# Optimization experiments

Hardware: AMD Instinct MI355X
Metric: run time of the kernel (lower is better)

Reference implementation:

```python
import jax, jax.numpy as jnp
import numpy as np

SCALING = 2.0  # alpha / r = 128 / 64


def setup_inputs() -> dict:
    key = jax.random.key(0)
    k1, k2, k3, k4, k5 = jax.random.split(key, 5)
    B, S, DIN, DOUT, R = 4, 2048, 4096, 4096, 64
    x = jax.random.normal(k1, (B, S, DIN), dtype=jnp.float32)
    # int8 quantized weight codes in [-127, 127] (stored as int32 for portability)
    qweight = jax.random.randint(k2, (DOUT, DIN), -127, 128, dtype=jnp.int32)
    # per-output-row absmax dequant scale (already divided by 127)
    scale = jax.random.uniform(k3, (DOUT, 1), dtype=jnp.float32, minval=0.005, maxval=0.02)
    lora_A = jax.random.normal(k4, (R, DIN), dtype=jnp.float32) * 0.02
    lora_B = jax.random.normal(k5, (DOUT, R), dtype=jnp.float32) * 0.02
    return {"x": x, "qweight": qweight, "scale": scale, "lora_A": lora_A, "lora_B": lora_B}


def reference(x, qweight, scale, lora_A, lora_B):
    # inline int8 dequant: w[o,i] = code[o,i] * scale[o]
    w = qweight.astype(x.dtype) * scale  # [DOUT, DIN]
    base = jnp.einsum('bsi,oi->bso', x, w)
    # low-rank LoRA path: (x @ A^T) @ B^T, scaled
    xa = jnp.einsum('bsi,ri->bsr', x, lora_A)       # [B,S,R]
    lora = jnp.einsum('bsr,or->bso', xa, lora_B)    # [B,S,DOUT]
    return base + SCALING * lora
```

## Files before the change

### kernel.cpp

```cpp
#include <hip/hip_runtime.h>
#include <hip/hip_bf16.h>
#include <stdint.h>


typedef __bf16 bf16x8 __attribute__((ext_vector_type(8)));
typedef float f32x4 __attribute__((ext_vector_type(4)));
typedef int i32x4 __attribute__((ext_vector_type(4)));

#define DIN   4096
#define DOUT  4096
#define MTOT  8192
#define RNK   64
#define NT    64
#define BUFB  24576

__device__ inline void gload_lds16(const void* g, void* l) {
  __builtin_amdgcn_global_load_lds((const __attribute__((address_space(1))) void*)g,
                                   (__attribute__((address_space(3))) void*)l,
                                   16, 0, 0);
}

__global__ __launch_bounds__(256) void quant_x_kernel(const float* __restrict__ x,
                                                      signed char* __restrict__ Xi8,
                                                      float* __restrict__ tstep) {
  const int row = blockIdx.x, t = threadIdx.x;
  const float4* xr = (const float4*)(x + (size_t)row * DIN);
  float4 v[4];
  float m = 0.f;
#pragma unroll
  for (int s = 0; s < 4; ++s) {
    v[s] = xr[t + s * 256];
    m = fmaxf(m, fmaxf(fmaxf(fabsf(v[s].x), fabsf(v[s].y)),
                       fmaxf(fabsf(v[s].z), fabsf(v[s].w))));
  }
#pragma unroll
  for (int off = 32; off > 0; off >>= 1) m = fmaxf(m, __shfl_xor(m, off));
  __shared__ float wm[4];
  if ((t & 63) == 0) wm[t >> 6] = m;
  __syncthreads();
  m = fmaxf(fmaxf(wm[0], wm[1]), fmaxf(wm[2], wm[3]));
  m = fmaxf(m, 1e-30f);
  const float rs = 127.0f / m;
  int* orow = (int*)(Xi8 + (size_t)row * DIN);
#pragma unroll
  for (int s = 0; s < 4; ++s) {
    float e[4] = {v[s].x, v[s].y, v[s].z, v[s].w};
    union { signed char c[4]; int i; } p;
#pragma unroll
    for (int j = 0; j < 4; ++j) {
      int q = __float2int_rn(e[j] * rs);
      q = q > 127 ? 127 : (q < -127 ? -127 : q);
      p.c[j] = (signed char)q;
    }
    orow[t + s * 256] = p.i;
  }
  if (t == 0) tstep[row] = m * (1.0f / 127.0f);
}

__global__ void cvt_w_kernel(const int* __restrict__ q, signed char* __restrict__ Wi8) {
  int i = blockIdx.x * blockDim.x + threadIdx.x;
  int4 v = ((const int4*)q)[i];
  union { signed char c[4]; int i; } p;
  p.c[0] = (signed char)v.x; p.c[1] = (signed char)v.y;
  p.c[2] = (signed char)v.z; p.c[3] = (signed char)v.w;
  ((int*)Wi8)[i] = p.i;
}

__global__ __launch_bounds__(256) void cvt_ab_kernel(const float* __restrict__ A,
                                                     const float* __restrict__ B,
                                                     signed char* __restrict__ Ai8,
                                                     float* __restrict__ astep,
                                                     __bf16* __restrict__ Blt) {
  const int t = threadIdx.x;
  if (blockIdx.x < 64) {
    const int row = blockIdx.x;
    const float4* ar = (const float4*)(A + (size_t)row * DIN);
    float4 v[4];
    float m = 0.f;
#pragma unroll
    for (int s = 0; s < 4; ++s) {
      v[s] = ar[t + s * 256];
      m = fmaxf(m, fmaxf(fmaxf(fabsf(v[s].x), fabsf(v[s].y)),
                         fmaxf(fabsf(v[s].z), fabsf(v[s].w))));
    }
#pragma unroll
    for (int off = 32; off > 0; off >>= 1) m = fmaxf(m, __shfl_xor(m, off));
    __shared__ float wm[4];
    if ((t & 63) == 0) wm[t >> 6] = m;
    __syncthreads();
    m = fmaxf(fmaxf(wm[0], wm[1]), fmaxf(wm[2], wm[3]));
    m = fmaxf(m, 1e-30f);
    const float rs = 127.0f / m;
    int* orow = (int*)(Ai8 + (size_t)row * DIN);
#pragma unroll
    for (int s = 0; s < 4; ++s) {
      float e[4] = {v[s].x, v[s].y, v[s].z, v[s].w};
      union { signed char c[4]; int i; } p;
#pragma unroll
      for (int j = 0; j < 4; ++j) {
        int q = __float2int_rn(e[j] * rs);
        q = q > 127 ? 127 : (q < -127 ? -127 : q);
        p.c[j] = (signed char)q;
      }
      orow[t + s * 256] = p.i;
    }
    if (t == 0) astep[row] = m * (1.0f / 127.0f);
  } else {
    int i = (blockIdx.x - 64) * 256 + t;
    float4 v = ((const float4*)B)[i];
    union { __bf16 h[4]; uint64_t u; } p;
    p.h[0] = (__bf16)(2.0f * v.x); p.h[1] = (__bf16)(2.0f * v.y);
    p.h[2] = (__bf16)(2.0f * v.z); p.h[3] = (__bf16)(2.0f * v.w);
    ((uint64_t*)Blt)[i] = p.u;
  }
}

__global__ __launch_bounds__(128) void lora_xa_kernel(const signed char* __restrict__ Xi8,
                                                      const float* __restrict__ tstep,
                                                      const signed char* __restrict__ Ai8,
                                                      const float* __restrict__ astep,
                                                      __bf16* __restrict__ xa) {
  int wid = threadIdx.x >> 6, lane = threadIdx.x & 63;
  int rowbase = blockIdx.x * 32 + wid * 16;
  i32x4 acc[4] = {};
  const signed char* xrow = Xi8 + (size_t)(rowbase + (lane & 15)) * DIN + (lane >> 4) * 16;
  const signed char* ab = Ai8 + (size_t)(lane & 15) * DIN + (lane >> 4) * 16;
  for (int k0 = 0; k0 < DIN; k0 += 64) {
    i32x4 af = *(const i32x4*)(xrow + k0);
#pragma unroll
    for (int ni = 0; ni < 4; ++ni) {
      i32x4 bv = *(const i32x4*)(ab + (size_t)ni * 16 * DIN + k0);
      acc[ni] = __builtin_amdgcn_mfma_i32_16x16x64_i8(af, bv, acc[ni], 0, 0, 0);
    }
  }
  f32x4 tm = *(const f32x4*)&tstep[rowbase + (lane >> 4) * 4];
#pragma unroll
  for (int ni = 0; ni < 4; ++ni) {
    const int col = ni * 16 + (lane & 15);
    const float as = astep[col];
#pragma unroll
    for (int j = 0; j < 4; ++j) {
      int row = rowbase + (lane >> 4) * 4 + j;
      xa[(size_t)row * RNK + col] = (__bf16)((float)acc[ni][j] * tm[j] * as);
    }
  }
}

__global__ __launch_bounds__(512, 4) void gemm_i8_kernel(const signed char* __restrict__ Xi8,
                                                         const signed char* __restrict__ Wi8,
                                                         const float* __restrict__ scale,
                                                         const float* __restrict__ tstep,
                                                         const __bf16* __restrict__ xa,
                                                         const __bf16* __restrict__ Blt,
                                                         float* __restrict__ out) {
  extern __shared__ char smem[];
  const int tid = threadIdx.x;
  const int lane = tid & 63;
  const int w = tid >> 6;
  const int wr = w >> 2;
  const int wc = w & 3;

  const int swz = (blockIdx.x & 7) * 128 + (blockIdx.x >> 3);
  const int bx = swz & 15;
  const int by = swz >> 4;
  const size_t bm = (size_t)by * 128, bn = (size_t)bx * 256;

  const int rc = ((lane >> 4) ^ ((lane >> 1) & 3)) << 4;
  const int srow = tid >> 2;
  const int scol = ((tid & 3) ^ ((tid >> 3) & 3)) << 4;

  auto SH = [&](const signed char* g, size_t r0, int srct, int ldsoff) {
    gload_lds16(g + (r0 + srow) * (size_t)4096 + srct * 64 + scol,
                smem + ldsoff + tid * 16);
  };
  auto stage = [&](int srct, int buf) {
    int b = buf * BUFB;
    SH(Xi8, bm, srct, b);
    SH(Wi8, bn, srct, b + 8192);
    SH(Wi8, bn + 128, srct, b + 16384);
  };

  const int aoff = (wr * 64 + (lane & 15)) * 64 + rc;
  const int boff = 8192 + (wc * 64 + (lane & 15)) * 64 + rc;

  i32x4 a[4], b[4];
  i32x4 acc[4][4] = {};

  stage(0, 0); stage(1, 1);
  asm volatile("s_waitcnt vmcnt(3)" ::: "memory");
  __builtin_amdgcn_s_barrier();

  int cur = 0;
  for (int kt = 0; kt < NT; ++kt) {
    const int bufb = cur * BUFB;
    if (kt < NT - 2) {
      int sb = cur + 2; if (sb >= 3) sb -= 3;
      stage(kt + 2, sb);
    }
#pragma unroll
    for (int mi = 0; mi < 4; ++mi)
      a[mi] = *(const i32x4*)(smem + bufb + aoff + mi * 1024);
#pragma unroll
    for (int ni = 0; ni < 4; ++ni)
      b[ni] = *(const i32x4*)(smem + bufb + boff + ni * 1024);
    __builtin_amdgcn_s_setprio(1);
#pragma unroll
    for (int mi = 0; mi < 4; ++mi)
#pragma unroll
      for (int ni = 0; ni < 4; ++ni)
        acc[mi][ni] = __builtin_amdgcn_mfma_i32_16x16x64_i8(a[mi], b[ni], acc[mi][ni], 0, 0, 0);
    __builtin_amdgcn_s_setprio(0);
    __builtin_amdgcn_sched_barrier(0);
    if (kt < NT - 2) { asm volatile("s_waitcnt vmcnt(3)" ::: "memory"); }
    else if (kt == NT - 2) { asm volatile("s_waitcnt vmcnt(0)" ::: "memory"); }
    __builtin_amdgcn_s_barrier();
    ++cur; if (cur >= 3) cur = 0;
  }

  const int sl_row = lane >> 3;
  const int sl_col = ((lane & 7) ^ (lane >> 3)) << 4;
  auto SBF = [&](const __bf16* g, size_t r0, int ldsoff) {
    char* d0 = smem + ldsoff + w * 2048 + lane * 16;
#pragma unroll
    for (int s = 0; s < 2; ++s) {
      const int rl = (w * 2 + s) * 8 + sl_row;
      gload_lds16((const char*)g + (r0 + rl) * 128 + sl_col, d0 + s * 1024);
    }
  };
  SBF(xa, bm, 0);
  SBF(Blt, bn, 16384); SBF(Blt, bn + 128, 32768);

  float sc[4];
#pragma unroll
  for (int ni = 0; ni < 4; ++ni)
    sc[ni] = scale[bn + wc * 64 + ni * 16 + (lane & 15)];

  asm volatile("s_waitcnt vmcnt(0)" ::: "memory");
  __builtin_amdgcn_s_barrier();

  const int cx0 = ((lane >> 4) << 4) ^ ((lane & 7) << 4);
  const int cx1 = (64 | ((lane >> 4) << 4)) ^ ((lane & 7) << 4);
  const int bltbase = 16384 + (wc >> 1) * 16384 + ((wc & 1) * 64 + (lane & 15)) * 128;

#pragma unroll
  for (int mi = 0; mi < 4; ++mi) {
    const int axb = (wr * 64 + mi * 16 + (lane & 15)) * 128;
    bf16x8 ax0 = *(const bf16x8*)(smem + axb + cx0);
    bf16x8 ax1 = *(const bf16x8*)(smem + axb + cx1);
    const size_t row = bm + wr * 64 + mi * 16 + (lane >> 4) * 4;
    f32x4 tm = *(const f32x4*)&tstep[row];
#pragma unroll
    for (int ni = 0; ni < 4; ++ni) {
      bf16x8 bl0 = *(const bf16x8*)(smem + bltbase + ni * 2048 + cx0);
      bf16x8 bl1 = *(const bf16x8*)(smem + bltbase + ni * 2048 + cx1);
      f32x4 l = {0.f, 0.f, 0.f, 0.f};
      l = __builtin_amdgcn_mfma_f32_16x16x32_bf16(ax0, bl0, l, 0, 0, 0);
      l = __builtin_amdgcn_mfma_f32_16x16x32_bf16(ax1, bl1, l, 0, 0, 0);
      const size_t col = bn + wc * 64 + ni * 16 + (lane & 15);
#pragma unroll
      for (int j = 0; j < 4; ++j)
        out[(row + j) * DOUT + col] = (float)acc[mi][ni][j] * (sc[ni] * tm[j]) + l[j];
    }
  }
}

extern "C" void kernel_launch(void* const* d_in, const int* in_sizes, int n_in,
                              void* d_out, int out_size, void* d_ws, size_t ws_size,
                              hipStream_t stream) {
  const float* x = (const float*)d_in[0];
  const int* qw = (const int*)d_in[1];
  const float* scale = (const float*)d_in[2];
  const float* lA = (const float*)d_in[3];
  const float* lB = (const float*)d_in[4];
  float* out = (float*)d_out;

  char* ws = (char*)d_ws;
  signed char* Xi8 = (signed char*)ws;
  signed char* Wi8 = (signed char*)(ws + 33554432);
  __bf16* xa    = (__bf16*)(ws + 50331648);
  signed char* Ai8 = (signed char*)(ws + 51380224);
  __bf16* Blt   = (__bf16*)(ws + 51904512);
  float* tstep  = (float*)(ws + 52428800);
  float* astep  = (float*)(ws + 52461568);

  hipFuncSetAttribute((const void*)gemm_i8_kernel,
                      hipFuncAttributeMaxDynamicSharedMemorySize, 3 * BUFB);

  quant_x_kernel<<<MTOT, 256, 0, stream>>>(x, Xi8, tstep);
  cvt_w_kernel<<<DOUT * (DIN / 4) / 256, 256, 0, stream>>>(qw, Wi8);
  cvt_ab_kernel<<<320, 256, 0, stream>>>(lA, lB, Ai8, astep, Blt);
  lora_xa_kernel<<<MTOT / 32, 128, 0, stream>>>(Xi8, tstep, Ai8, astep, xa);
  gemm_i8_kernel<<<(MTOT / 128) * (DOUT / 256), 512, 3 * BUFB, stream>>>(
      Xi8, Wi8, scale, tstep, xa, Blt, out);
}
```

Baseline: 222.8 us.

## Enlarge GEMM tile to 256x256 with 32x32 MFMA and fuse prep kernels

The int8 GEMM block tile grows from 128x256 to 256x256, and the 16x16x64 MFMAs become 32x32x32 i8 MFMAs with 16-wide accumulators. This raises arithmetic intensity per LDS read and halves the block count. The LoRA epilogue is rewritten to use 32x32x16 bf16 MFMAs over the larger tile. The three preprocessing kernels (x quantization, weight int32-to-int8 conversion, A/B conversion) are merged into one launch to cut launch overhead. Costs are more LDS per block (96KB) and more registers, with occupancy bounds relaxed to one block per CU.

```diff
diff --git a/kernel.cpp b/kernel.cpp
--- a/kernel.cpp
+++ b/kernel.cpp
@@ -5,14 +5,16 @@
 
 typedef __bf16 bf16x8 __attribute__((ext_vector_type(8)));
 typedef float f32x4 __attribute__((ext_vector_type(4)));
+typedef float f32x16 __attribute__((ext_vector_type(16)));
 typedef int i32x4 __attribute__((ext_vector_type(4)));
+typedef int i32x16 __attribute__((ext_vector_type(16)));
 
 #define DIN   4096
 #define DOUT  4096
 #define MTOT  8192
 #define RNK   64
 #define NT    64
-#define BUFB  24576
+#define BUFB  32768
 
 __device__ inline void gload_lds16(const void* g, void* l) {
   __builtin_amdgcn_global_load_lds((const __attribute__((address_space(1))) void*)g,
@@ -20,66 +22,30 @@
                                    16, 0, 0);
 }
 
-__global__ __launch_bounds__(256) void quant_x_kernel(const float* __restrict__ x,
-                                                      signed char* __restrict__ Xi8,
-                                                      float* __restrict__ tstep) {
-  const int row = blockIdx.x, t = threadIdx.x;
-  const float4* xr = (const float4*)(x + (size_t)row * DIN);
-  float4 v[4];
-  float m = 0.f;
-#pragma unroll
-  for (int s = 0; s < 4; ++s) {
-    v[s] = xr[t + s * 256];
-    m = fmaxf(m, fmaxf(fmaxf(fabsf(v[s].x), fabsf(v[s].y)),
-                       fmaxf(fabsf(v[s].z), fabsf(v[s].w))));
-  }
-#pragma unroll
-  for (int off = 32; off > 0; off >>= 1) m = fmaxf(m, __shfl_xor(m, off));
-  __shared__ float wm[4];
-  if ((t & 63) == 0) wm[t >> 6] = m;
-  __syncthreads();
-  m = fmaxf(fmaxf(wm[0], wm[1]), fmaxf(wm[2], wm[3]));
-  m = fmaxf(m, 1e-30f);
-  const float rs = 127.0f / m;
-  int* orow = (int*)(Xi8 + (size_t)row * DIN);
-#pragma unroll
-  for (int s = 0; s < 4; ++s) {
-    float e[4] = {v[s].x, v[s].y, v[s].z, v[s].w};
-    union { signed char c[4]; int i; } p;
-#pragma unroll
-    for (int j = 0; j < 4; ++j) {
-      int q = __float2int_rn(e[j] * rs);
-      q = q > 127 ? 127 : (q < -127 ? -127 : q);
-      p.c[j] = (signed char)q;
-    }
-    orow[t + s * 256] = p.i;
-  }
-  if (t == 0) tstep[row] = m * (1.0f / 127.0f);
-}
-
-__global__ void cvt_w_kernel(const int* __restrict__ q, signed char* __restrict__ Wi8) {
-  int i = blockIdx.x * blockDim.x + threadIdx.x;
-  int4 v = ((const int4*)q)[i];
-  union { signed char c[4]; int i; } p;
-  p.c[0] = (signed char)v.x; p.c[1] = (signed char)v.y;
-  p.c[2] = (signed char)v.z; p.c[3] = (signed char)v.w;
-  ((int*)Wi8)[i] = p.i;
-}
-
-__global__ __launch_bounds__(256) void cvt_ab_kernel(const float* __restrict__ A,
-                                                     const float* __restrict__ B,
-                                                     signed char* __restrict__ Ai8,
-                                                     float* __restrict__ astep,
-                                                     __bf16* __restrict__ Blt) {
-  const int t = threadIdx.x;
-  if (blockIdx.x < 64) {
-    const int row = blockIdx.x;
-    const float4* ar = (const float4*)(A + (size_t)row * DIN);
+__global__ __launch_bounds__(256) void prep_kernel(const float* __restrict__ x,
+                                                   const int* __restrict__ qw,
+                                                   const float* __restrict__ lA,
+                                                   const float* __restrict__ lB,
+                                                   signed char* __restrict__ Xi8,
+                                                   float* __restrict__ tstep,
+                                                   signed char* __restrict__ Wi8,
+                                                   signed char* __restrict__ Ai8,
+                                                   float* __restrict__ astep,
+                                                   __bf16* __restrict__ Blt) {
+  const int bid = blockIdx.x, t = threadIdx.x;
+  const float* src = nullptr;
+  signed char* dst = nullptr;
+  float* stp = nullptr;
+  int row = 0;
+  if (bid < 8192) { src = x; dst = Xi8; stp = tstep; row = bid; }
+  else if (bid < 8256) { src = lA; dst = Ai8; stp = astep; row = bid - 8192; }
+  if (src) {
+    const float4* xr = (const float4*)(src + (size_t)row * DIN);
     float4 v[4];
     float m = 0.f;
 #pragma unroll
     for (int s = 0; s < 4; ++s) {
-      v[s] = ar[t + s * 256];
+      v[s] = xr[t + s * 256];
       m = fmaxf(m, fmaxf(fmaxf(fabsf(v[s].x), fabsf(v[s].y)),
                          fmaxf(fabsf(v[s].z), fabsf(v[s].w))));
     }
@@ -91,7 +57,7 @@
     m = fmaxf(fmaxf(wm[0], wm[1]), fmaxf(wm[2], wm[3]));
     m = fmaxf(m, 1e-30f);
     const float rs = 127.0f / m;
-    int* orow = (int*)(Ai8 + (size_t)row * DIN);
+    int* orow = (int*)(dst + (size_t)row * DIN);
 #pragma unroll
     for (int s = 0; s < 4; ++s) {
       float e[4] = {v[s].x, v[s].y, v[s].z, v[s].w};
@@ -104,14 +70,21 @@
       }
       orow[t + s * 256] = p.i;
     }
-    if (t == 0) astep[row] = m * (1.0f / 127.0f);
-  } else {
-    int i = (blockIdx.x - 64) * 256 + t;
-    float4 v = ((const float4*)B)[i];
+    if (t == 0) stp[row] = m * (1.0f / 127.0f);
+  } else if (bid < 8512) {
+    int i = (bid - 8256) * 256 + t;
+    float4 v = ((const float4*)lB)[i];
     union { __bf16 h[4]; uint64_t u; } p;
     p.h[0] = (__bf16)(2.0f * v.x); p.h[1] = (__bf16)(2.0f * v.y);
     p.h[2] = (__bf16)(2.0f * v.z); p.h[3] = (__bf16)(2.0f * v.w);
     ((uint64_t*)Blt)[i] = p.u;
+  } else {
+    int i = (bid - 8512) * 256 + t;
+    int4 v = ((const int4*)qw)[i];
+    union { signed char c[4]; int i; } p;
+    p.c[0] = (signed char)v.x; p.c[1] = (signed char)v.y;
+    p.c[2] = (signed char)v.z; p.c[3] = (signed char)v.w;
+    ((int*)Wi8)[i] = p.i;
   }
 }
 
@@ -146,7 +119,7 @@
   }
 }
 
-__global__ __launch_bounds__(512, 4) void gemm_i8_kernel(const signed char* __restrict__ Xi8,
+__global__ __launch_bounds__(512, 1) void gemm_i8_kernel(const signed char* __restrict__ Xi8,
                                                          const signed char* __restrict__ Wi8,
                                                          const float* __restrict__ scale,
                                                          const float* __restrict__ tstep,
@@ -160,12 +133,11 @@
   const int wr = w >> 2;
   const int wc = w & 3;
 
-  const int swz = (blockIdx.x & 7) * 128 + (blockIdx.x >> 3);
+  const int swz = (blockIdx.x & 7) * 64 + (blockIdx.x >> 3);
   const int bx = swz & 15;
   const int by = swz >> 4;
-  const size_t bm = (size_t)by * 128, bn = (size_t)bx * 256;
-
-  const int rc = ((lane >> 4) ^ ((lane >> 1) & 3)) << 4;
+  const size_t bm = (size_t)by * 256, bn = (size_t)bx * 256;
+
   const int srow = tid >> 2;
   const int scol = ((tid & 3) ^ ((tid >> 3) & 3)) << 4;
 
@@ -175,19 +147,20 @@
   };
   auto stage = [&](int srct, int buf) {
     int b = buf * BUFB;
-    SH(Xi8, bm, srct, b);
-    SH(Wi8, bn, srct, b + 8192);
-    SH(Wi8, bn + 128, srct, b + 16384);
+    SH(Xi8, bm, srct, b); SH(Xi8, bm + 128, srct, b + 8192);
+    SH(Wi8, bn, srct, b + 16384); SH(Wi8, bn + 128, srct, b + 24576);
   };
 
-  const int aoff = (wr * 64 + (lane & 15)) * 64 + rc;
-  const int boff = 8192 + (wc * 64 + (lane & 15)) * 64 + rc;
-
-  i32x4 a[4], b[4];
-  i32x4 acc[4][4] = {};
+  const int lr64 = (lane & 31) * 64;
+  const int lx = (lane >> 1) & 3;
+  const int sl0 = ((0 * 2 + (lane >> 5)) ^ lx) << 4;
+  const int sl1 = ((1 * 2 + (lane >> 5)) ^ lx) << 4;
+
+  i32x4 a[4][2], b[2][2];
+  i32x16 acc[4][2] = {};
 
   stage(0, 0); stage(1, 1);
-  asm volatile("s_waitcnt vmcnt(3)" ::: "memory");
+  asm volatile("s_waitcnt vmcnt(4)" ::: "memory");
   __builtin_amdgcn_s_barrier();
 
   int cur = 0;
@@ -197,69 +170,78 @@
       int sb = cur + 2; if (sb >= 3) sb -= 3;
       stage(kt + 2, sb);
     }
-#pragma unroll
-    for (int mi = 0; mi < 4; ++mi)
-      a[mi] = *(const i32x4*)(smem + bufb + aoff + mi * 1024);
-#pragma unroll
-    for (int ni = 0; ni < 4; ++ni)
-      b[ni] = *(const i32x4*)(smem + bufb + boff + ni * 1024);
+    const int ab = bufb + wr * 128 * 64 + lr64;
+    const int bb = bufb + 16384 + wc * 64 * 64 + lr64;
+#pragma unroll
+    for (int mi = 0; mi < 4; ++mi) {
+      a[mi][0] = *(const i32x4*)(smem + ab + mi * 2048 + sl0);
+      a[mi][1] = *(const i32x4*)(smem + ab + mi * 2048 + sl1);
+    }
+#pragma unroll
+    for (int ni = 0; ni < 2; ++ni) {
+      b[ni][0] = *(const i32x4*)(smem + bb + ni * 2048 + sl0);
+      b[ni][1] = *(const i32x4*)(smem + bb + ni * 2048 + sl1);
+    }
     __builtin_amdgcn_s_setprio(1);
 #pragma unroll
-    for (int mi = 0; mi < 4; ++mi)
-#pragma unroll
-      for (int ni = 0; ni < 4; ++ni)
-        acc[mi][ni] = __builtin_amdgcn_mfma_i32_16x16x64_i8(a[mi], b[ni], acc[mi][ni], 0, 0, 0);
+    for (int ks = 0; ks < 2; ++ks)
+#pragma unroll
+      for (int mi = 0; mi < 4; ++mi)
+#pragma unroll
+        for (int ni = 0; ni < 2; ++ni)
+          acc[mi][ni] = __builtin_amdgcn_mfma_i32_32x32x32_i8(a[mi][ks], b[ni][ks], acc[mi][ni], 0, 0, 0);
     __builtin_amdgcn_s_setprio(0);
     __builtin_amdgcn_sched_barrier(0);
-    if (kt < NT - 2) { asm volatile("s_waitcnt vmcnt(3)" ::: "memory"); }
+    if (kt < NT - 2) { asm volatile("s_waitcnt vmcnt(4)" ::: "memory"); }
     else if (kt == NT - 2) { asm volatile("s_waitcnt vmcnt(0)" ::: "memory"); }
     __builtin_amdgcn_s_barrier();
     ++cur; if (cur >= 3) cur = 0;
   }
 
-  const int sl_row = lane >> 3;
-  const int sl_col = ((lane & 7) ^ (lane >> 3)) << 4;
+  const int erow = tid >> 3;
+  const int ecol = (((tid & 7) ^ ((tid >> 3) & 7)) << 4);
   auto SBF = [&](const __bf16* g, size_t r0, int ldsoff) {
-    char* d0 = smem + ldsoff + w * 2048 + lane * 16;
-#pragma unroll
-    for (int s = 0; s < 2; ++s) {
-      const int rl = (w * 2 + s) * 8 + sl_row;
-      gload_lds16((const char*)g + (r0 + rl) * 128 + sl_col, d0 + s * 1024);
-    }
+    gload_lds16((const char*)g + (r0 + erow) * 128 + ecol, smem + ldsoff + tid * 16);
   };
-  SBF(xa, bm, 0);
-  SBF(Blt, bn, 16384); SBF(Blt, bn + 128, 32768);
-
-  float sc[4];
-#pragma unroll
-  for (int ni = 0; ni < 4; ++ni)
-    sc[ni] = scale[bn + wc * 64 + ni * 16 + (lane & 15)];
+  SBF(xa, bm, 0); SBF(xa, bm + 64, 8192);
+  SBF(xa, bm + 128, 16384); SBF(xa, bm + 192, 24576);
+  SBF(Blt, bn, 32768); SBF(Blt, bn + 64, 40960);
+  SBF(Blt, bn + 128, 49152); SBF(Blt, bn + 192, 57344);
+
+  const float sc0 = scale[bn + wc * 64 + (lane & 31)];
+  const float sc1 = scale[bn + wc * 64 + 32 + (lane & 31)];
 
   asm volatile("s_waitcnt vmcnt(0)" ::: "memory");
   __builtin_amdgcn_s_barrier();
 
-  const int cx0 = ((lane >> 4) << 4) ^ ((lane & 7) << 4);
-  const int cx1 = (64 | ((lane >> 4) << 4)) ^ ((lane & 7) << 4);
-  const int bltbase = 16384 + (wc >> 1) * 16384 + ((wc & 1) * 64 + (lane & 15)) * 128;
-
+  const int exr = lane & 7;
+  const int lr128 = (lane & 31) * 128;
 #pragma unroll
   for (int mi = 0; mi < 4; ++mi) {
-    const int axb = (wr * 64 + mi * 16 + (lane & 15)) * 128;
-    bf16x8 ax0 = *(const bf16x8*)(smem + axb + cx0);
-    bf16x8 ax1 = *(const bf16x8*)(smem + axb + cx1);
-    const size_t row = bm + wr * 64 + mi * 16 + (lane >> 4) * 4;
-    f32x4 tm = *(const f32x4*)&tstep[row];
-#pragma unroll
-    for (int ni = 0; ni < 4; ++ni) {
-      bf16x8 bl0 = *(const bf16x8*)(smem + bltbase + ni * 2048 + cx0);
-      bf16x8 bl1 = *(const bf16x8*)(smem + bltbase + ni * 2048 + cx1);
-      f32x4 l = {0.f, 0.f, 0.f, 0.f};
-      l = __builtin_amdgcn_mfma_f32_16x16x32_bf16(ax0, bl0, l, 0, 0, 0);
-      l = __builtin_amdgcn_mfma_f32_16x16x32_bf16(ax1, bl1, l, 0, 0, 0);
-      const size_t col = bn + wc * 64 + ni * 16 + (lane & 15);
-#pragma unroll
-      for (int j = 0; j < 4; ++j)
-        out[(row + j) * DOUT + col] = (float)acc[mi][ni][j] * (sc[ni] * tm[j]) + l[j];
+    const int arow0 = wr * 128 + mi * 32;
+    const int abase = arow0 * 128 + lr128;
+    f32x4 tm[4];
+#pragma unroll
+    for (int g = 0; g < 4; ++g)
+      tm[g] = *(const f32x4*)&tstep[bm + arow0 + 8 * g + 4 * (lane >> 5)];
+#pragma unroll
+    for (int ni = 0; ni < 2; ++ni) {
+      const int bbase = 32768 + (wc * 64 + ni * 32) * 128 + lr128;
+      f32x16 l = {};
+#pragma unroll
+      for (int ks = 0; ks < 4; ++ks) {
+        const int sl = ((2 * ks + (lane >> 5)) ^ exr) << 4;
+        bf16x8 ax = *(const bf16x8*)(smem + abase + sl);
+        bf16x8 bl = *(const bf16x8*)(smem + bbase + sl);
+        l = __builtin_amdgcn_mfma_f32_32x32x16_bf16(ax, bl, l, 0, 0, 0);
+      }
+      const float scn = ni ? sc1 : sc0;
+      const size_t col = bn + wc * 64 + ni * 32 + (lane & 31);
+#pragma unroll
+      for (int reg = 0; reg < 16; ++reg) {
+        const size_t row = bm + arow0 + (reg & 3) + 8 * (reg >> 2) + 4 * (lane >> 5);
+        out[row * DOUT + col] = (float)acc[mi][ni][reg] * (scn * tm[reg >> 2][reg & 3]) + l[reg];
+      }
     }
   }
 }
@@ -286,10 +268,8 @@
   hipFuncSetAttribute((const void*)gemm_i8_kernel,
                       hipFuncAttributeMaxDynamicSharedMemorySize, 3 * BUFB);
 
-  quant_x_kernel<<<MTOT, 256, 0, stream>>>(x, Xi8, tstep);
-  cvt_w_kernel<<<DOUT * (DIN / 4) / 256, 256, 0, stream>>>(qw, Wi8);
-  cvt_ab_kernel<<<320, 256, 0, stream>>>(lA, lB, Ai8, astep, Blt);
+  prep_kernel<<<24896, 256, 0, stream>>>(x, qw, lA, lB, Xi8, tstep, Wi8, Ai8, astep, Blt);
   lora_xa_kernel<<<MTOT / 32, 128, 0, stream>>>(Xi8, tstep, Ai8, astep, xa);
-  gemm_i8_kernel<<<(MTOT / 128) * (DOUT / 256), 512, 3 * BUFB, stream>>>(
+  gemm_i8_kernel<<<(MTOT / 256) * (DOUT / 256), 512, 3 * BUFB, stream>>>(
       Xi8, Wi8, scale, tstep, xa, Blt, out);
 }
```

New measurement: 225.3 us. About the same (+1.1%).
